# Performance work log

Hardware: AMD Instinct MI355X
Metric: run time of the kernel (lower is better)

Reference implementation:

```python
import jax, jax.numpy as jnp
import numpy as np

BLOCK_SIZE = 16
MASK_TOKEN_ID = 31999
D_MODEL = 2048
N_HEADS = 16
VOCAB = 32000
NEG = -1e30


def setup_inputs() -> dict:
    key = jax.random.key(0)
    ks = jax.random.split(key, 8)
    B, S, D, V = 1, 1024, D_MODEL, VOCAB
    sd = 1.0 / np.sqrt(D)
    return {
        "input_ids": jax.random.randint(ks[0], (B, S), 0, V),
        "attention_mask": jnp.ones((B, S), dtype=jnp.float32),
        "hidden_states": jax.random.normal(ks[1], (B, S, D), dtype=jnp.float32),
        "loss_mask": jnp.ones((B, S), dtype=jnp.float32),
        "embed_table": jax.random.normal(ks[2], (V, D), dtype=jnp.float32) * 0.02,
        "Wq": jax.random.normal(ks[3], (D, D), dtype=jnp.float32) * sd,
        "Wk": jax.random.normal(ks[4], (D, D), dtype=jnp.float32) * sd,
        "Wv": jax.random.normal(ks[5], (D, D), dtype=jnp.float32) * sd,
        "Wo": jax.random.normal(ks[6], (D, D), dtype=jnp.float32) * sd,
        "lm_head_w": jax.random.normal(ks[7], (D, V), dtype=jnp.float32) * sd,
    }


def reference(input_ids, attention_mask, hidden_states, loss_mask,
              embed_table, Wq, Wk, Wv, Wo, lm_head_w):
    B, S = input_ids.shape
    bs = BLOCK_SIZE
    L = (S // bs) * bs  # effective_len
    input_ids = input_ids[:, :L]
    hidden_states = hidden_states[:, :L, :]
    loss_mask = loss_mask[:, :L]

    positions = jnp.arange(L)
    is_block_start = positions % bs == 0
    block_ids = positions // bs

    # noise input: first token of each block real, rest MASK
    noise_ids = jnp.where(is_block_start[None, :], input_ids, MASK_TOKEN_ID)
    noise_emb = embed_table[noise_ids]  # [B, L, D]

    # [L, 2L] DFlash mask: ctx kv visible if its block < q block; noise kv if same block
    ctx_vis = block_ids[None, :] < block_ids[:, None]
    noise_vis = block_ids[:, None] == block_ids[None, :]
    full_mask = jnp.concatenate([ctx_vis, noise_vis], axis=1)  # [L, 2L] bool

    # draft attention: q from noise tokens, kv over [target_hidden ; noise]
    H = N_HEADS
    hd = hidden_states.shape[-1] // H
    kv_in = jnp.concatenate([hidden_states, noise_emb], axis=1)  # [B, 2L, D]
    q = (noise_emb @ Wq).reshape(B, L, H, hd).transpose(0, 2, 1, 3)      # [B,H,L,hd]
    k = (kv_in @ Wk).reshape(B, 2 * L, H, hd).transpose(0, 2, 1, 3)      # [B,H,2L,hd]
    v = (kv_in @ Wv).reshape(B, 2 * L, H, hd).transpose(0, 2, 1, 3)
    scores = jnp.einsum("bhqd,bhkd->bhqk", q, k) / jnp.sqrt(jnp.float32(hd))
    scores = jnp.where(full_mask[None, None, :, :], scores, NEG)
    attn = jax.nn.softmax(scores, axis=-1)
    ctx = jnp.einsum("bhqk,bhkd->bhqd", attn, v)
    hidden = ctx.transpose(0, 2, 1, 3).reshape(B, L, -1) @ Wo  # [B, L, D]

    logits = hidden @ lm_head_w  # [B, L, V]

    # dflash loss mask: exclude first block and block starts (gamma=None)
    is_first_block = block_ids == 0
    valid = (~is_first_block) & (~is_block_start)
    combined = loss_mask * valid.astype(jnp.float32)  # [B, L]
    active = combined > 1e-6

    logp = jax.nn.log_softmax(logits, axis=-1)
    ce = -jnp.take_along_axis(logp, input_ids[..., None], axis=-1)[..., 0]  # [B, L]
    count = jnp.sum(active.astype(jnp.float32))
    loss = jnp.sum(jnp.where(active, ce, 0.0)) / count

    preds = jnp.argmax(logits, axis=-1)
    correct = jnp.sum(jnp.where(active, (preds == input_ids).astype(jnp.float32), 0.0))
    accuracy = correct / count
    return loss, accuracy
```

## Files before the change

kernel.cpp:

```cpp
#include <hip/hip_runtime.h>

typedef unsigned int uint32;
typedef unsigned short u16;
typedef __attribute__((ext_vector_type(8))) short bf16x8;
typedef __attribute__((ext_vector_type(4))) float f32x4;

__device__ __forceinline__ u16 f2b(float f) {
  uint32 u = __float_as_uint(f);
  u = (u + 0x7fffu + ((u >> 16) & 1u)) >> 16;
  return (u16)u;
}
__device__ __forceinline__ float b2f(u16 h) {
  return __uint_as_float(((uint32)h) << 16);
}
__device__ __forceinline__ void gl_lds16(const void* g, void* l) {
  typedef const __attribute__((address_space(1))) void* gp_t;
  typedef __attribute__((address_space(3))) void* lp_t;
  __builtin_amdgcn_global_load_lds((gp_t)g, (lp_t)l, 16, 0, 0);
}

#define L 1024
#define D 2048
#define NH 16
#define HD 128
#define VOCAB 32000
#define KV 2048
#define MASK_ID 31999

static constexpr long OFF_KV  = 0;
static constexpr long OFF_WTQ = OFF_KV  + 8388608;
static constexpr long OFF_WTK = OFF_WTQ + 8388608;
static constexpr long OFF_WTV = OFF_WTK + 8388608;
static constexpr long OFF_WTO = OFF_WTV + 8388608;
static constexpr long OFF_Q   = OFF_WTO + 8388608;
static constexpr long OFF_K   = OFF_Q   + 4194304;
static constexpr long OFF_VT  = OFF_K   + 8388608;
static constexpr long OFF_CTX = OFF_VT  + 8388608;
static constexpr long OFF_HID = OFF_CTX + 4194304;
static constexpr long OFF_LMT = OFF_HID + 4194304;
static constexpr long OFF_PM  = OFF_LMT + 131072000;
static constexpr long OFF_PS  = OFF_PM  + 524288;
static constexpr long OFF_PI  = OFF_PS  + 524288;
static constexpr long OFF_PT  = OFF_PI  + 524288;
static constexpr long OFF_ROW = OFF_PT  + 4096;
static constexpr long WS_NEED = OFF_ROW + 8192;

__global__ __launch_bounds__(256) void prep_kv(const float* __restrict__ hs,
                                               const int* __restrict__ ids,
                                               const float* __restrict__ emb,
                                               u16* __restrict__ kv) {
  int r = blockIdx.x;
  int t = threadIdx.x;
  const float* src;
  if (r < L) {
    src = hs + (long)r * D;
  } else {
    int p = r - L;
    int id = ((p & 15) == 0) ? ids[p] : MASK_ID;
    src = emb + (long)id * D;
  }
  float4 a = *(const float4*)(src + t * 8);
  float4 b = *(const float4*)(src + t * 8 + 4);
  u16* dst = kv + (long)r * D + t * 8;
  ushort4 o0, o1;
  o0.x = f2b(a.x); o0.y = f2b(a.y); o0.z = f2b(a.z); o0.w = f2b(a.w);
  o1.x = f2b(b.x); o1.y = f2b(b.y); o1.z = f2b(b.z); o1.w = f2b(b.w);
  *(ushort4*)dst = o0;
  *(ushort4*)(dst + 4) = o1;
}

__device__ __forceinline__ void transpose_body(const float* __restrict__ W,
                                               u16* __restrict__ WT,
                                               int Kd, int Nd) {
  __shared__ float tile[128 * 129];
  int n0 = blockIdx.x * 128;
  int k0 = blockIdx.y * 128;
  int t = threadIdx.x;
  int r = t >> 5;
  int c4 = (t & 31) * 4;
#pragma unroll
  for (int p = 0; p < 16; ++p) {
    int kk = p * 8 + r;
    float4 v = *(const float4*)(W + (long)(k0 + kk) * Nd + n0 + c4);
    float* dst = tile + kk * 129 + c4;
    dst[0] = v.x; dst[1] = v.y; dst[2] = v.z; dst[3] = v.w;
  }
  __syncthreads();
#pragma unroll
  for (int p = 0; p < 16; ++p) {
    int nn = p * 8 + r;
    ushort4 o;
    o.x = f2b(tile[(c4 + 0) * 129 + nn]);
    o.y = f2b(tile[(c4 + 1) * 129 + nn]);
    o.z = f2b(tile[(c4 + 2) * 129 + nn]);
    o.w = f2b(tile[(c4 + 3) * 129 + nn]);
    *(ushort4*)(WT + (long)(n0 + nn) * Kd + k0 + c4) = o;
  }
}

__global__ __launch_bounds__(256) void transpose_conv(const float* __restrict__ W,
                                                      u16* __restrict__ WT,
                                                      int Kd, int Nd) {
  transpose_body(W, WT, Kd, Nd);
}

__global__ __launch_bounds__(256) void transpose4(const float* __restrict__ W0, const float* __restrict__ W1,
                                                  const float* __restrict__ W2, const float* __restrict__ W3,
                                                  u16* __restrict__ T0, u16* __restrict__ T1,
                                                  u16* __restrict__ T2, u16* __restrict__ T3) {
  int z = blockIdx.z;
  const float* W = (z == 0) ? W0 : (z == 1) ? W1 : (z == 2) ? W2 : W3;
  u16* T = (z == 0) ? T0 : (z == 1) ? T1 : (z == 2) ? T2 : T3;
  transpose_body(W, T, D, D);
}

#define EPI_PLAIN 0
#define EPI_QKV 3
#define EPI_CE 4

template <int EPI>
__global__ __launch_bounds__(256) void gemm128(const u16* __restrict__ A, int lda, long aHead,
                                               const u16* __restrict__ BT, int ldb, long bHead,
                                               u16* __restrict__ C, int ldc, long cHead,
                                               int Kd) {
  __shared__ __align__(16) char lds[16384];
  char* a_lds = lds;
  char* b_lds = lds + 8192;
  int tid = threadIdx.x;
  int lane = tid & 63;
  int wave = tid >> 6;
  int wr = wave >> 1, wc = wave & 1;
  int h = blockIdx.z;
  long tm = (long)blockIdx.x * 128;
  long tn = (long)blockIdx.y * 128;
  const u16* Ap = A + (long)h * aHead + tm * lda;
  const u16* Bp = BT + (long)h * bHead + tn * ldb;

  int soff = tid * 16;
  int srow = soff >> 6;
  int scol = (soff & 63) >> 1;
  char* aldsb = a_lds + wave * 1024;
  char* bldsb = b_lds + wave * 1024;

  f32x4 acc[4][4];
#pragma unroll
  for (int i = 0; i < 4; ++i)
#pragma unroll
    for (int j = 0; j < 4; ++j) acc[i][j] = (f32x4){0.f, 0.f, 0.f, 0.f};

  for (int k0 = 0; k0 < Kd; k0 += 32) {
#pragma unroll
    for (int r = 0; r < 2; ++r) {
      gl_lds16(Ap + (long)(srow + r * 64) * lda + k0 + scol, aldsb + r * 4096);
      gl_lds16(Bp + (long)(srow + r * 64) * ldb + k0 + scol, bldsb + r * 4096);
    }
    __syncthreads();
    bf16x8 af[4], bfr[4];
    int ka = (lane >> 4) << 4;
#pragma unroll
    for (int mi = 0; mi < 4; ++mi)
      af[mi] = *(const bf16x8*)(a_lds + (wr * 64 + mi * 16 + (lane & 15)) * 64 + ka);
#pragma unroll
    for (int ni = 0; ni < 4; ++ni)
      bfr[ni] = *(const bf16x8*)(b_lds + (wc * 64 + ni * 16 + (lane & 15)) * 64 + ka);
#pragma unroll
    for (int mi = 0; mi < 4; ++mi)
#pragma unroll
      for (int ni = 0; ni < 4; ++ni)
        acc[mi][ni] = __builtin_amdgcn_mfma_f32_16x16x32_bf16(af[mi], bfr[ni], acc[mi][ni], 0, 0, 0);
    __syncthreads();
  }

  long crow0 = tm + wr * 64 + ((lane >> 4) << 2);
  int ccol0 = wc * 64 + (lane & 15);
  u16* Cp = C + (long)h * cHead;
#pragma unroll
  for (int mi = 0; mi < 4; ++mi) {
#pragma unroll
    for (int ni = 0; ni < 4; ++ni) {
      long col = tn + ccol0 + ni * 16;
#pragma unroll
      for (int j = 0; j < 4; ++j) {
        long row = crow0 + mi * 16 + j;
        Cp[row * ldc + col] = f2b(acc[mi][ni][j]);
      }
    }
  }
}

template <int EPI>
__global__ __launch_bounds__(512, 2) void gemm256(const u16* __restrict__ A, int lda,
                                                  const u16* __restrict__ BT, int ldb,
                                                  u16* __restrict__ C, int ldc,
                                                  int Kd, int mtiles,
                                                  u16* __restrict__ Cq, u16* __restrict__ Ck,
                                                  u16* __restrict__ Cv,
                                                  const int* __restrict__ ids,
                                                  float* __restrict__ PMAX,
                                                  float* __restrict__ PSUM,
                                                  int* __restrict__ PARGI,
                                                  float* __restrict__ PTGT) {
  __shared__ __align__(16) char lds[131072];
  int nwg = gridDim.x;
  int orig = blockIdx.x;
  int q8 = nwg >> 3, r8 = nwg & 7;
  int xcd = orig & 7, idx = orig >> 3;
  int wg = (xcd < r8 ? xcd * (q8 + 1) : r8 * (q8 + 1) + (xcd - r8) * q8) + idx;
  int tm, tn;
  if (EPI == EPI_QKV) {
    if (wg < 32) { tn = wg >> 2; tm = 4 + (wg & 3); }
    else { int e = wg - 32; tn = 8 + (e >> 3); tm = e & 7; }
  } else {
    tm = wg % mtiles; tn = wg / mtiles;
  }

  int tid = threadIdx.x, lane = tid & 63, w = tid >> 6;
  int wm = w >> 2, wn = w & 3;
  const u16* Ap = A + (long)tm * 256 * lda;
  const u16* Bp = BT + (long)tn * 256 * ldb;
  int NT = Kd >> 6;
  int maxs = NT << 2;

  auto STAGE_SLOT = [&](int s) {
    if (s >= maxs) return;
    int tau = s >> 2, hh = s & 3;
    int kind = (hh & 1) ^ 1;
    int ks = hh >> 1;
    const u16* src = kind ? Bp : Ap;
    int ld = kind ? ldb : lda;
    char* dst0 = lds + (tau & 1) * 65536 + kind * 32768 + ks * 16384;
    long kbase = (long)tau * 64 + ks * 32;
#pragma unroll
    for (int l = 0; l < 2; ++l) {
      int o = tid * 16 + l * 8192;
      int rr = o >> 6;
      int ch = (o >> 4) & 3;
      int clog = ch ^ ((rr >> 1) & 3);
      gl_lds16(src + (long)rr * ld + kbase + clog * 8, dst0 + w * 1024 + l * 8192);
    }
  };
  auto LDA = [&](int tau, int ks, int mi) -> bf16x8 {
    int rr = wm * 128 + mi * 16 + (lane & 15);
    int qq = lane >> 4;
    return *(const bf16x8*)(lds + (tau & 1) * 65536 + ks * 16384 + rr * 64 +
                            ((qq ^ ((rr >> 1) & 3)) << 4));
  };
  auto LDB = [&](int tau, int ks, int ni) -> bf16x8 {
    int rr = wn * 64 + ni * 16 + (lane & 15);
    int qq = lane >> 4;
    return *(const bf16x8*)(lds + (tau & 1) * 65536 + 32768 + ks * 16384 + rr * 64 +
                            ((qq ^ ((rr >> 1) & 3)) << 4));
  };

  f32x4 acc[8][4];
#pragma unroll
  for (int i = 0; i < 8; ++i)
#pragma unroll
    for (int j = 0; j < 4; ++j) acc[i][j] = (f32x4){0.f, 0.f, 0.f, 0.f};

  STAGE_SLOT(0); STAGE_SLOT(1); STAGE_SLOT(2); STAGE_SLOT(3);
  asm volatile("s_waitcnt vmcnt(4)" ::: "memory");
  STAGE_SLOT(4); STAGE_SLOT(5); STAGE_SLOT(6);
  asm volatile("s_waitcnt vmcnt(6)" ::: "memory");
  __builtin_amdgcn_s_barrier();
  __builtin_amdgcn_sched_barrier(0);

  bf16x8 bfr[4];

#define G256_PHASE(TAU, KS, MH, SLOT, WAITV)                                   \
  {                                                                            \
    bf16x8 af[4];                                                              \
    if (MH == 0) {                                                             \
      bfr[0] = LDB(TAU, KS, 0); bfr[1] = LDB(TAU, KS, 1);                      \
      bfr[2] = LDB(TAU, KS, 2); bfr[3] = LDB(TAU, KS, 3);                      \
    }                                                                          \
    af[0] = LDA(TAU, KS, MH * 4 + 0); af[1] = LDA(TAU, KS, MH * 4 + 1);        \
    af[2] = LDA(TAU, KS, MH * 4 + 2); af[3] = LDA(TAU, KS, MH * 4 + 3);        \
    STAGE_SLOT(SLOT);                                                          \
    __builtin_amdgcn_sched_barrier(0);                                         \
    __builtin_amdgcn_s_barrier();                                              \
    asm volatile("s_waitcnt lgkmcnt(0)" ::: "memory");                         \
    __builtin_amdgcn_sched_barrier(0);                                         \
    __builtin_amdgcn_s_setprio(1);                                             \
    _Pragma("unroll")                                                          \
    for (int mi2 = 0; mi2 < 4; ++mi2)                                          \
      _Pragma("unroll")                                                        \
      for (int ni = 0; ni < 4; ++ni)                                           \
        acc[MH * 4 + mi2][ni] = __builtin_amdgcn_mfma_f32_16x16x32_bf16(       \
            af[mi2], bfr[ni], acc[MH * 4 + mi2][ni], 0, 0, 0);                 \
    __builtin_amdgcn_s_setprio(0);                                             \
    __builtin_amdgcn_sched_barrier(0);                                         \
    if (WAITV == 6) asm volatile("s_waitcnt vmcnt(6)" ::: "memory");           \
    else if (WAITV == 0) asm volatile("s_waitcnt vmcnt(0)" ::: "memory");      \
    __builtin_amdgcn_s_barrier();                                              \
    __builtin_amdgcn_sched_barrier(0);                                         \
  }

  for (int t = 0; t < NT; t += 2) {
    int s0 = 4 * t;
    int w4 = (t + 2 >= NT) ? 0 : 6;
    G256_PHASE(t,     0, 0, s0 + 7,  -1)
    G256_PHASE(t,     0, 1, s0 + 8,  -1)
    G256_PHASE(t,     1, 0, s0 + 9,  -1)
    G256_PHASE(t,     1, 1, s0 + 10, w4)
    G256_PHASE(t + 1, 0, 0, s0 + 11, -1)
    G256_PHASE(t + 1, 0, 1, s0 + 12, -1)
    G256_PHASE(t + 1, 1, 0, s0 + 13, -1)
    G256_PHASE(t + 1, 1, 1, s0 + 14, 6)
  }
#undef G256_PHASE

  if (EPI == EPI_CE) {
    __syncthreads();
    float* smax = (float*)lds;
    float* ssum = smax + 1024;
    int* sargi = (int*)(ssum + 1024);
    int lq = lane & 15, qq = lane >> 4;
#pragma unroll
    for (int mi = 0; mi < 8; ++mi) {
#pragma unroll
      for (int j = 0; j < 4; ++j) {
        int lrow = mi * 16 + qq * 4 + j;
        long grow = (long)tm * 256 + wm * 128 + lrow;
        int tgt = ids[grow];
        float v[4];
        float mx = -1e30f; int ai = 0;
#pragma unroll
        for (int ni = 0; ni < 4; ++ni) {
          v[ni] = acc[mi][ni][j];
          int col = tn * 256 + wn * 64 + ni * 16 + lq;
          if (col == tgt) PTGT[grow] = v[ni];
          if (v[ni] > mx) { mx = v[ni]; ai = col; }
        }
#pragma unroll
        for (int off = 1; off < 16; off <<= 1) {
          float om = __shfl_xor(mx, off);
          int oa = __shfl_xor(ai, off);
          if (om > mx || (om == mx && oa < ai)) { mx = om; ai = oa; }
        }
        float se = 0.f;
#pragma unroll
        for (int ni = 0; ni < 4; ++ni) se += __expf(v[ni] - mx);
#pragma unroll
        for (int off = 1; off < 16; off <<= 1) se += __shfl_xor(se, off);
        if (lq == 0) {
          int f = wm * 128 + lrow;
          smax[f * 4 + wn] = mx;
          ssum[f * 4 + wn] = se;
          sargi[f * 4 + wn] = ai;
        }
      }
    }
    __syncthreads();
    if (lane < 32) {
      int f = w * 32 + lane;
      float m_t = smax[f * 4]; int a_t = sargi[f * 4];
#pragma unroll
      for (int x = 1; x < 4; ++x) {
        float om = smax[f * 4 + x]; int oa = sargi[f * 4 + x];
        if (om > m_t || (om == m_t && oa < a_t)) { m_t = om; a_t = oa; }
      }
      float s_t = 0.f;
#pragma unroll
      for (int x = 0; x < 4; ++x) s_t += ssum[f * 4 + x] * __expf(smax[f * 4 + x] - m_t);
      long grow = (long)tm * 256 + f;
      PMAX[grow * 128 + tn] = m_t;
      PSUM[grow * 128 + tn] = s_t;
      PARGI[grow * 128 + tn] = a_t;
    }
    return;
  }

  long crow = (long)tm * 256 + wm * 128 + ((lane >> 4) << 2);
  long ccol = (long)tn * 256 + wn * 64 + (lane & 15);
#pragma unroll
  for (int mi = 0; mi < 8; ++mi)
#pragma unroll
    for (int ni = 0; ni < 4; ++ni)
#pragma unroll
      for (int j = 0; j < 4; ++j) {
        long row = crow + mi * 16 + j;
        long col = ccol + ni * 16;
        u16 val = f2b(acc[mi][ni][j]);
        if (EPI == EPI_PLAIN) {
          C[row * ldc + col] = val;
        } else {
          if (col < 2048) {
            if (row >= 1024) Cq[(row - 1024) * D + col] = val;
          } else if (col < 4096) {
            Ck[row * D + (col - 2048)] = val;
          } else {
            Cv[(col - 4096) * KV + row] = val;
          }
        }
      }
}

__global__ __launch_bounds__(256) void ce_combine(const float* __restrict__ PMAX,
                                                  const float* __restrict__ PSUM,
                                                  const int* __restrict__ PARGI,
                                                  const float* __restrict__ PTGT,
                                                  const int* __restrict__ ids,
                                                  float* __restrict__ rowbuf) {
  int row = blockIdx.x * 4 + (threadIdx.x >> 6);
  int lane = threadIdx.x & 63;
  const float* pm = PMAX + (long)row * 128;
  const float* ps = PSUM + (long)row * 128;
  const int* pi = PARGI + (long)row * 128;
  float m0 = (lane < 125) ? pm[lane] : -1e30f;
  int a0 = (lane < 125) ? pi[lane] : (1 << 30);
  float m1 = (lane + 64 < 125) ? pm[lane + 64] : -1e30f;
  int a1 = (lane + 64 < 125) ? pi[lane + 64] : (1 << 30);
  float mg = m0; int ag = a0;
  if (m1 > mg || (m1 == mg && a1 < ag)) { mg = m1; ag = a1; }
  for (int off = 1; off < 64; off <<= 1) {
    float om = __shfl_xor(mg, off);
    int oa = __shfl_xor(ag, off);
    if (om > mg || (om == mg && oa < ag)) { mg = om; ag = oa; }
  }
  float s = 0.f;
  if (lane < 125) s += ps[lane] * __expf(m0 - mg);
  if (lane + 64 < 125) s += ps[lane + 64] * __expf(m1 - mg);
  for (int off = 1; off < 64; off <<= 1) s += __shfl_xor(s, off);
  if (lane == 0) {
    rowbuf[row * 2] = mg + logf(s) - PTGT[row];
    rowbuf[row * 2 + 1] = (ag == ids[row]) ? 1.f : 0.f;
  }
}

__global__ __launch_bounds__(256) void flash_attn(const u16* __restrict__ qb,
                                                  const u16* __restrict__ kb,
                                                  const u16* __restrict__ vt,
                                                  u16* __restrict__ ctx) {
  int tid = threadIdx.x;
  int lane = tid & 63;
  int wid = blockIdx.x * 4 + (tid >> 6);
  int pairid = wid >> 1;
  int h = pairid >> 5;
  int pr = pairid & 31;
  int rb = (wid & 1) ? (63 - pr) : pr;
  int lq = lane & 15;
  int g = lane >> 4;
  const float scale = 0.08838834764831845f;

  const u16* qrow = qb + (long)(rb * 16 + lq) * D + h * HD + g * 8;
  bf16x8 qf[4];
#pragma unroll
  for (int c = 0; c < 4; ++c) qf[c] = *(const bf16x8*)(qrow + c * 32);

  f32x4 o[8];
#pragma unroll
  for (int i = 0; i < 8; ++i) o[i] = (f32x4){0.f, 0.f, 0.f, 0.f};
  float m = -1e30f, lsum = 0.f;

  int nb = rb + 1;
  for (int bp = 0; bp < nb; bp += 2) {
    bool validB = (bp + 1) < nb;
    int tokA = (bp < rb) ? bp * 16 : 1024 + rb * 16;
    int bB = bp + 1;
    int tokB = validB ? ((bB < rb) ? bB * 16 : 1024 + rb * 16) : tokA;

    f32x4 sA = (f32x4){0.f, 0.f, 0.f, 0.f};
    f32x4 sB = (f32x4){0.f, 0.f, 0.f, 0.f};
    const u16* ka = kb + (long)(tokA + lq) * D + h * HD + g * 8;
#pragma unroll
    for (int c = 0; c < 4; ++c) {
      bf16x8 kf = *(const bf16x8*)(ka + c * 32);
      sA = __builtin_amdgcn_mfma_f32_16x16x32_bf16(kf, qf[c], sA, 0, 0, 0);
    }
    if (validB) {
      const u16* kbp = kb + (long)(tokB + lq) * D + h * HD + g * 8;
#pragma unroll
      for (int c = 0; c < 4; ++c) {
        bf16x8 kf = *(const bf16x8*)(kbp + c * 32);
        sB = __builtin_amdgcn_mfma_f32_16x16x32_bf16(kf, qf[c], sB, 0, 0, 0);
      }
    }

    float s8[8];
#pragma unroll
    for (int j = 0; j < 4; ++j) s8[j] = sA[j] * scale;
#pragma unroll
    for (int j = 0; j < 4; ++j) s8[4 + j] = validB ? sB[j] * scale : -1e30f;
    float mx = s8[0];
#pragma unroll
    for (int j = 1; j < 8; ++j) mx = fmaxf(mx, s8[j]);
    mx = fmaxf(mx, __shfl_xor(mx, 16));
    mx = fmaxf(mx, __shfl_xor(mx, 32));
    float mn = fmaxf(m, mx);
    float sc_f = __expf(m - mn);
    m = mn;
    float p[8], ps = 0.f;
#pragma unroll
    for (int j = 0; j < 8; ++j) { p[j] = __expf(s8[j] - mn); ps += p[j]; }
    ps += __shfl_xor(ps, 16);
    ps += __shfl_xor(ps, 32);
    lsum = lsum * sc_f + ps;

    uint32 Aw0 = (uint32)f2b(p[0]) | ((uint32)f2b(p[1]) << 16);
    uint32 Aw1 = (uint32)f2b(p[2]) | ((uint32)f2b(p[3]) << 16);
    uint32 Bw0 = (uint32)f2b(p[4]) | ((uint32)f2b(p[5]) << 16);
    uint32 Bw1 = (uint32)f2b(p[6]) | ((uint32)f2b(p[7]) << 16);
    int s0 = (((2 * g) & 3) << 4) + lq;
    int s1 = (((2 * g + 1) & 3) << 4) + lq;
    uint32 a00 = (uint32)__shfl((int)Aw0, s0), a01 = (uint32)__shfl((int)Aw1, s0);
    uint32 a10 = (uint32)__shfl((int)Aw0, s1), a11 = (uint32)__shfl((int)Aw1, s1);
    uint32 b00 = (uint32)__shfl((int)Bw0, s0), b01 = (uint32)__shfl((int)Bw1, s0);
    uint32 b10 = (uint32)__shfl((int)Bw0, s1), b11 = (uint32)__shfl((int)Bw1, s1);
    union { uint32 u[4]; bf16x8 v; } pu;
    pu.u[0] = (g < 2) ? a00 : b00;
    pu.u[1] = (g < 2) ? a01 : b01;
    pu.u[2] = (g < 2) ? a10 : b10;
    pu.u[3] = (g < 2) ? a11 : b11;

#pragma unroll
    for (int nt = 0; nt < 8; ++nt)
#pragma unroll
      for (int j = 0; j < 4; ++j) o[nt][j] *= sc_f;
    int tok_g = (g < 2) ? (tokA + g * 8) : (tokB + (g - 2) * 8);
    const u16* vrow = vt + (long)(h * HD + lq) * KV + tok_g;
#pragma unroll
    for (int nt = 0; nt < 8; ++nt) {
      bf16x8 vf = *(const bf16x8*)(vrow + (long)nt * 16 * KV);
      o[nt] = __builtin_amdgcn_mfma_f32_16x16x32_bf16(vf, pu.v, o[nt], 0, 0, 0);
    }
  }

  float inv = 1.f / lsum;
  u16* cp = ctx + (long)(rb * 16 + lq) * D + h * HD + g * 4;
#pragma unroll
  for (int nt = 0; nt < 8; ++nt) {
    ushort4 st;
    st.x = f2b(o[nt][0] * inv); st.y = f2b(o[nt][1] * inv);
    st.z = f2b(o[nt][2] * inv); st.w = f2b(o[nt][3] * inv);
    *(ushort4*)(cp + nt * 16) = st;
  }
}

__global__ __launch_bounds__(256) void final_reduce(const float* __restrict__ rowbuf,
                                                    const float* __restrict__ loss_mask,
                                                    float* __restrict__ out) {
  int t = threadIdx.x;
  float ce = 0.f, cnt = 0.f, cor = 0.f;
  for (int r = t; r < L; r += 256) {
    bool valid = (r >= 16) && ((r & 15) != 0);
    float comb = loss_mask[r] * (valid ? 1.f : 0.f);
    if (comb > 1e-6f) {
      ce += rowbuf[r * 2];
      cor += rowbuf[r * 2 + 1];
      cnt += 1.f;
    }
  }
  for (int off = 1; off < 64; off <<= 1) {
    ce += __shfl_xor(ce, off);
    cnt += __shfl_xor(cnt, off);
    cor += __shfl_xor(cor, off);
  }
  __shared__ float s1[4], s2[4], s3[4];
  int lane = t & 63, w = t >> 6;
  if (lane == 0) { s1[w] = ce; s2[w] = cnt; s3[w] = cor; }
  __syncthreads();
  if (t == 0) {
    float C = s1[0] + s1[1] + s1[2] + s1[3];
    float N = s2[0] + s2[1] + s2[2] + s2[3];
    float R = s3[0] + s3[1] + s3[2] + s3[3];
    out[0] = C / N;
    out[1] = R / N;
  }
}

__global__ void ws_too_small(float* out, float mb) {
  if (threadIdx.x == 0) { out[0] = 1e6f + mb; out[1] = -1e6f; }
}

extern "C" void kernel_launch(void* const* d_in, const int* in_sizes, int n_in,
                              void* d_out, int out_size, void* d_ws, size_t ws_size,
                              hipStream_t stream) {
  const int* ids = (const int*)d_in[0];
  const float* hs = (const float*)d_in[2];
  const float* lmask = (const float*)d_in[3];
  const float* emb = (const float*)d_in[4];
  const float* Wq = (const float*)d_in[5];
  const float* Wk = (const float*)d_in[6];
  const float* Wv = (const float*)d_in[7];
  const float* Wo = (const float*)d_in[8];
  const float* Wlm = (const float*)d_in[9];
  float* out = (float*)d_out;
  char* ws = (char*)d_ws;

  if (ws_size < (size_t)WS_NEED) {
    ws_too_small<<<1, 64, 0, stream>>>(out, (float)(ws_size >> 20));
    return;
  }

  u16* kv  = (u16*)(ws + OFF_KV);
  u16* wtq = (u16*)(ws + OFF_WTQ);
  u16* wtk = (u16*)(ws + OFF_WTK);
  u16* wtv = (u16*)(ws + OFF_WTV);
  u16* wto = (u16*)(ws + OFF_WTO);
  u16* qb  = (u16*)(ws + OFF_Q);
  u16* kb  = (u16*)(ws + OFF_K);
  u16* vt  = (u16*)(ws + OFF_VT);
  u16* ctx = (u16*)(ws + OFF_CTX);
  u16* hid = (u16*)(ws + OFF_HID);
  u16* lmt = (u16*)(ws + OFF_LMT);
  float* PMAX = (float*)(ws + OFF_PM);
  float* PSUM = (float*)(ws + OFF_PS);
  int* PARGI = (int*)(ws + OFF_PI);
  float* PTGT = (float*)(ws + OFF_PT);
  float* rowbuf = (float*)(ws + OFF_ROW);

  prep_kv<<<2048, 256, 0, stream>>>(hs, ids, emb, kv);
  transpose4<<<dim3(16, 16, 4), 256, 0, stream>>>(Wq, Wk, Wv, Wo, wtq, wtk, wtv, wto);
  transpose_conv<<<dim3(250, 16), 256, 0, stream>>>(Wlm, lmt, D, VOCAB);

  gemm256<EPI_QKV><<<dim3(160), 512, 0, stream>>>(kv, D, wtq, D, nullptr, 0, D, 0,
                                                  qb, kb, vt,
                                                  nullptr, nullptr, nullptr, nullptr, nullptr);

  flash_attn<<<dim3(256), 256, 0, stream>>>(qb, kb, vt, ctx);

  gemm128<EPI_PLAIN><<<dim3(8, 16, 1), 256, 0, stream>>>(ctx, D, 0, wto, D, 0, hid, D, 0, D);

  gemm256<EPI_CE><<<dim3(500), 512, 0, stream>>>(hid, D, lmt, D, nullptr, 0, D, 4,
                                                 nullptr, nullptr, nullptr,
                                                 ids, PMAX, PSUM, PARGI, PTGT);

  ce_combine<<<256, 256, 0, stream>>>(PMAX, PSUM, PARGI, PTGT, ids, rowbuf);
  final_reduce<<<1, 256, 0, stream>>>(rowbuf, lmask, out);
}
```

Measured before the change: 465.3 us.

## Merge prep and transposes into one launch, overlap LM-head transpose with QKV GEMM

The kv conversion and the four DxD weight transposes now run in a single 512-thread launch. A second launch runs the QKV GEMM (160 workgroups) alongside a grid-stride transpose of the LM-head weight on the remaining 352 workgroups, so the bandwidth-bound transpose overlaps compute-bound GEMM work. The GEMM body also precomputes its LDS fragment pointers and global staging offsets instead of recomputing addresses in each phase. The costs are idle-block imbalance between the two roles and a 128KB LDS allocation for the transpose blocks, which lowers their occupancy.

```diff
diff --git a/kernel.cpp b/kernel.cpp
--- a/kernel.cpp
+++ b/kernel.cpp
@@ -45,73 +45,70 @@
 static constexpr long OFF_ROW = OFF_PT  + 4096;
 static constexpr long WS_NEED = OFF_ROW + 8192;
 
-__global__ __launch_bounds__(256) void prep_kv(const float* __restrict__ hs,
-                                               const int* __restrict__ ids,
-                                               const float* __restrict__ emb,
-                                               u16* __restrict__ kv) {
-  int r = blockIdx.x;
+__device__ __forceinline__ void transpose128(float* tile, const float* __restrict__ W,
+                                             u16* __restrict__ WT,
+                                             int Kd, int Nd, int k0, int n0) {
   int t = threadIdx.x;
-  const float* src;
-  if (r < L) {
-    src = hs + (long)r * D;
+  int r = t >> 2, cq = (t & 3) * 4;
+#pragma unroll
+  for (int p = 0; p < 8; ++p) {
+    int c = cq + p * 16;
+    float4 v = *(const float4*)(W + (long)(k0 + r) * Nd + n0 + c);
+    float* d = tile + r * 129 + c;
+    d[0] = v.x; d[1] = v.y; d[2] = v.z; d[3] = v.w;
+  }
+  __syncthreads();
+  int q = t & 15, nn0 = t >> 4;
+#pragma unroll
+  for (int p = 0; p < 4; ++p) {
+    int nn = nn0 + p * 32;
+    union { u16 v[8]; bf16x8 b; } u;
+#pragma unroll
+    for (int j = 0; j < 8; ++j) u.v[j] = f2b(tile[(q * 8 + j) * 129 + nn]);
+    *(bf16x8*)(WT + (long)(n0 + nn) * Kd + k0 + q * 8) = u.b;
+  }
+}
+
+__global__ __launch_bounds__(512) void mega1(const float* __restrict__ hs,
+                                             const int* __restrict__ ids,
+                                             const float* __restrict__ emb,
+                                             u16* __restrict__ kv,
+                                             const float* __restrict__ Wq, const float* __restrict__ Wk,
+                                             const float* __restrict__ Wv, const float* __restrict__ Wo,
+                                             u16* __restrict__ wtq, u16* __restrict__ wtk,
+                                             u16* __restrict__ wtv, u16* __restrict__ wto) {
+  __shared__ float tile[128 * 129];
+  int bid = blockIdx.x;
+  int t = threadIdx.x;
+  if (bid < 512) {
+    int r = bid * 4 + (t >> 7);
+    int c0 = (t & 127) * 16;
+    const float* src;
+    if (r < L) {
+      src = hs + (long)r * D;
+    } else {
+      int p = r - L;
+      int id = ((p & 15) == 0) ? ids[p] : MASK_ID;
+      src = emb + (long)id * D;
+    }
+    u16* dst = kv + (long)r * D + c0;
+#pragma unroll
+    for (int qy = 0; qy < 2; ++qy) {
+      float4 a = *(const float4*)(src + c0 + qy * 8);
+      float4 b = *(const float4*)(src + c0 + qy * 8 + 4);
+      ushort4 o0, o1;
+      o0.x = f2b(a.x); o0.y = f2b(a.y); o0.z = f2b(a.z); o0.w = f2b(a.w);
+      o1.x = f2b(b.x); o1.y = f2b(b.y); o1.z = f2b(b.z); o1.w = f2b(b.w);
+      *(ushort4*)(dst + qy * 8) = o0;
+      *(ushort4*)(dst + qy * 8 + 4) = o1;
+    }
   } else {
-    int p = r - L;
-    int id = ((p & 15) == 0) ? ids[p] : MASK_ID;
-    src = emb + (long)id * D;
-  }
-  float4 a = *(const float4*)(src + t * 8);
-  float4 b = *(const float4*)(src + t * 8 + 4);
-  u16* dst = kv + (long)r * D + t * 8;
-  ushort4 o0, o1;
-  o0.x = f2b(a.x); o0.y = f2b(a.y); o0.z = f2b(a.z); o0.w = f2b(a.w);
-  o1.x = f2b(b.x); o1.y = f2b(b.y); o1.z = f2b(b.z); o1.w = f2b(b.w);
-  *(ushort4*)dst = o0;
-  *(ushort4*)(dst + 4) = o1;
-}
-
-__device__ __forceinline__ void transpose_body(const float* __restrict__ W,
-                                               u16* __restrict__ WT,
-                                               int Kd, int Nd) {
-  __shared__ float tile[128 * 129];
-  int n0 = blockIdx.x * 128;
-  int k0 = blockIdx.y * 128;
-  int t = threadIdx.x;
-  int r = t >> 5;
-  int c4 = (t & 31) * 4;
-#pragma unroll
-  for (int p = 0; p < 16; ++p) {
-    int kk = p * 8 + r;
-    float4 v = *(const float4*)(W + (long)(k0 + kk) * Nd + n0 + c4);
-    float* dst = tile + kk * 129 + c4;
-    dst[0] = v.x; dst[1] = v.y; dst[2] = v.z; dst[3] = v.w;
-  }
-  __syncthreads();
-#pragma unroll
-  for (int p = 0; p < 16; ++p) {
-    int nn = p * 8 + r;
-    ushort4 o;
-    o.x = f2b(tile[(c4 + 0) * 129 + nn]);
-    o.y = f2b(tile[(c4 + 1) * 129 + nn]);
-    o.z = f2b(tile[(c4 + 2) * 129 + nn]);
-    o.w = f2b(tile[(c4 + 3) * 129 + nn]);
-    *(ushort4*)(WT + (long)(n0 + nn) * Kd + k0 + c4) = o;
-  }
-}
-
-__global__ __launch_bounds__(256) void transpose_conv(const float* __restrict__ W,
-                                                      u16* __restrict__ WT,
-                                                      int Kd, int Nd) {
-  transpose_body(W, WT, Kd, Nd);
-}
-
-__global__ __launch_bounds__(256) void transpose4(const float* __restrict__ W0, const float* __restrict__ W1,
-                                                  const float* __restrict__ W2, const float* __restrict__ W3,
-                                                  u16* __restrict__ T0, u16* __restrict__ T1,
-                                                  u16* __restrict__ T2, u16* __restrict__ T3) {
-  int z = blockIdx.z;
-  const float* W = (z == 0) ? W0 : (z == 1) ? W1 : (z == 2) ? W2 : W3;
-  u16* T = (z == 0) ? T0 : (z == 1) ? T1 : (z == 2) ? T2 : T3;
-  transpose_body(W, T, D, D);
+    int idx = bid - 512;
+    int z = idx >> 8, tt = idx & 255;
+    const float* W = (z == 0) ? Wq : (z == 1) ? Wk : (z == 2) ? Wv : Wo;
+    u16* T = (z == 0) ? wtq : (z == 1) ? wtk : (z == 2) ? wtv : wto;
+    transpose128(tile, W, T, D, D, (tt >> 4) * 128, (tt & 15) * 128);
+  }
 }
 
 #define EPI_PLAIN 0
@@ -189,23 +186,15 @@
 }
 
 template <int EPI>
-__global__ __launch_bounds__(512, 2) void gemm256(const u16* __restrict__ A, int lda,
-                                                  const u16* __restrict__ BT, int ldb,
-                                                  u16* __restrict__ C, int ldc,
-                                                  int Kd, int mtiles,
-                                                  u16* __restrict__ Cq, u16* __restrict__ Ck,
-                                                  u16* __restrict__ Cv,
-                                                  const int* __restrict__ ids,
-                                                  float* __restrict__ PMAX,
-                                                  float* __restrict__ PSUM,
-                                                  int* __restrict__ PARGI,
-                                                  float* __restrict__ PTGT) {
-  __shared__ __align__(16) char lds[131072];
-  int nwg = gridDim.x;
-  int orig = blockIdx.x;
-  int q8 = nwg >> 3, r8 = nwg & 7;
-  int xcd = orig & 7, idx = orig >> 3;
-  int wg = (xcd < r8 ? xcd * (q8 + 1) : r8 * (q8 + 1) + (xcd - r8) * q8) + idx;
+__device__ __forceinline__ void gemm256_body(char* lds, int wg,
+                                             const u16* __restrict__ A, int lda,
+                                             const u16* __restrict__ BT,
+                                             int Kd, int mtiles,
+                                             u16* __restrict__ Cq, u16* __restrict__ Ck,
+                                             u16* __restrict__ Cv,
+                                             const int* __restrict__ ids,
+                                             float* __restrict__ PMAX, float* __restrict__ PSUM,
+                                             int* __restrict__ PARGI, float* __restrict__ PTGT) {
   int tm, tn;
   if (EPI == EPI_QKV) {
     if (wg < 32) { tn = wg >> 2; tm = 4 + (wg & 3); }
@@ -216,40 +205,39 @@
 
   int tid = threadIdx.x, lane = tid & 63, w = tid >> 6;
   int wm = w >> 2, wn = w & 3;
-  const u16* Ap = A + (long)tm * 256 * lda;
-  const u16* Bp = BT + (long)tn * 256 * ldb;
+  int lq = lane & 15, qq = lane >> 4;
+  const char* Ap = (const char*)(A + (long)tm * 256 * lda);
+  const char* Bp = (const char*)(BT + (long)tn * 256 * lda);
   int NT = Kd >> 6;
   int maxs = NT << 2;
+
+  int swz = qq ^ ((lq >> 1) & 3);
+  char* pA0 = lds + ((wm * 128 + lq) * 64 + (swz << 4));
+  char* pA1 = pA0 + 65536;
+  char* pB0 = lds + 32768 + ((wn * 64 + lq) * 64 + (swz << 4));
+  char* pB1 = pB0 + 65536;
+  int voff[2], lof[2];
+#pragma unroll
+  for (int l = 0; l < 2; ++l) {
+    int o = tid * 16 + l * 8192;
+    int rr = o >> 6;
+    int ch = (o >> 4) & 3;
+    int clog = ch ^ ((rr >> 1) & 3);
+    voff[l] = (rr * lda + clog * 8) * 2;
+    lof[l] = w * 1024 + l * 8192;
+  }
 
   auto STAGE_SLOT = [&](int s) {
     if (s >= maxs) return;
     int tau = s >> 2, hh = s & 3;
     int kind = (hh & 1) ^ 1;
     int ks = hh >> 1;
-    const u16* src = kind ? Bp : Ap;
-    int ld = kind ? ldb : lda;
-    char* dst0 = lds + (tau & 1) * 65536 + kind * 32768 + ks * 16384;
-    long kbase = (long)tau * 64 + ks * 32;
-#pragma unroll
-    for (int l = 0; l < 2; ++l) {
-      int o = tid * 16 + l * 8192;
-      int rr = o >> 6;
-      int ch = (o >> 4) & 3;
-      int clog = ch ^ ((rr >> 1) & 3);
-      gl_lds16(src + (long)rr * ld + kbase + clog * 8, dst0 + w * 1024 + l * 8192);
-    }
-  };
-  auto LDA = [&](int tau, int ks, int mi) -> bf16x8 {
-    int rr = wm * 128 + mi * 16 + (lane & 15);
-    int qq = lane >> 4;
-    return *(const bf16x8*)(lds + (tau & 1) * 65536 + ks * 16384 + rr * 64 +
-                            ((qq ^ ((rr >> 1) & 3)) << 4));
-  };
-  auto LDB = [&](int tau, int ks, int ni) -> bf16x8 {
-    int rr = wn * 64 + ni * 16 + (lane & 15);
-    int qq = lane >> 4;
-    return *(const bf16x8*)(lds + (tau & 1) * 65536 + 32768 + ks * 16384 + rr * 64 +
-                            ((qq ^ ((rr >> 1) & 3)) << 4));
+    const char* src = kind ? Bp : Ap;
+    long kb = (long)tau * 128 + ks * 64;
+    char* dstb = lds + (tau & 1) * 65536 + kind * 32768 + ks * 16384;
+#pragma unroll
+    for (int l = 0; l < 2; ++l)
+      gl_lds16(src + kb + voff[l], dstb + lof[l]);
   };
 
   f32x4 acc[8][4];
@@ -267,15 +255,19 @@
 
   bf16x8 bfr[4];
 
-#define G256_PHASE(TAU, KS, MH, SLOT, WAITV)                                   \
+#define G256_PHASE(PA, PB, KS, MH, SLOT, WAITV)                                \
   {                                                                            \
     bf16x8 af[4];                                                              \
     if (MH == 0) {                                                             \
-      bfr[0] = LDB(TAU, KS, 0); bfr[1] = LDB(TAU, KS, 1);                      \
-      bfr[2] = LDB(TAU, KS, 2); bfr[3] = LDB(TAU, KS, 3);                      \
+      bfr[0] = *(const bf16x8*)((PB) + (KS) * 16384 + 0 * 1024);               \
+      bfr[1] = *(const bf16x8*)((PB) + (KS) * 16384 + 1 * 1024);               \
+      bfr[2] = *(const bf16x8*)((PB) + (KS) * 16384 + 2 * 1024);               \
+      bfr[3] = *(const bf16x8*)((PB) + (KS) * 16384 + 3 * 1024);               \
     }                                                                          \
-    af[0] = LDA(TAU, KS, MH * 4 + 0); af[1] = LDA(TAU, KS, MH * 4 + 1);        \
-    af[2] = LDA(TAU, KS, MH * 4 + 2); af[3] = LDA(TAU, KS, MH * 4 + 3);        \
+    af[0] = *(const bf16x8*)((PA) + (KS) * 16384 + (MH * 4 + 0) * 1024);       \
+    af[1] = *(const bf16x8*)((PA) + (KS) * 16384 + (MH * 4 + 1) * 1024);       \
+    af[2] = *(const bf16x8*)((PA) + (KS) * 16384 + (MH * 4 + 2) * 1024);       \
+    af[3] = *(const bf16x8*)((PA) + (KS) * 16384 + (MH * 4 + 3) * 1024);       \
     STAGE_SLOT(SLOT);                                                          \
     __builtin_amdgcn_sched_barrier(0);                                         \
     __builtin_amdgcn_s_barrier();                                              \
@@ -299,14 +291,14 @@
   for (int t = 0; t < NT; t += 2) {
     int s0 = 4 * t;
     int w4 = (t + 2 >= NT) ? 0 : 6;
-    G256_PHASE(t,     0, 0, s0 + 7,  -1)
-    G256_PHASE(t,     0, 1, s0 + 8,  -1)
-    G256_PHASE(t,     1, 0, s0 + 9,  -1)
-    G256_PHASE(t,     1, 1, s0 + 10, w4)
-    G256_PHASE(t + 1, 0, 0, s0 + 11, -1)
-    G256_PHASE(t + 1, 0, 1, s0 + 12, -1)
-    G256_PHASE(t + 1, 1, 0, s0 + 13, -1)
-    G256_PHASE(t + 1, 1, 1, s0 + 14, 6)
+    G256_PHASE(pA0, pB0, 0, 0, s0 + 7,  -1)
+    G256_PHASE(pA0, pB0, 0, 1, s0 + 8,  -1)
+    G256_PHASE(pA0, pB0, 1, 0, s0 + 9,  -1)
+    G256_PHASE(pA0, pB0, 1, 1, s0 + 10, w4)
+    G256_PHASE(pA1, pB1, 0, 0, s0 + 11, -1)
+    G256_PHASE(pA1, pB1, 0, 1, s0 + 12, -1)
+    G256_PHASE(pA1, pB1, 1, 0, s0 + 13, -1)
+    G256_PHASE(pA1, pB1, 1, 1, s0 + 14, 6)
   }
 #undef G256_PHASE
 
@@ -315,7 +307,6 @@
     float* smax = (float*)lds;
     float* ssum = smax + 1024;
     int* sargi = (int*)(ssum + 1024);
-    int lq = lane & 15, qq = lane >> 4;
 #pragma unroll
     for (int mi = 0; mi < 8; ++mi) {
 #pragma unroll
@@ -372,7 +363,7 @@
   }
 
   long crow = (long)tm * 256 + wm * 128 + ((lane >> 4) << 2);
-  long ccol = (long)tn * 256 + wn * 64 + (lane & 15);
+  long ccol = (long)tn * 256 + wn * 64 + lq;
 #pragma unroll
   for (int mi = 0; mi < 8; ++mi)
 #pragma unroll
@@ -382,18 +373,51 @@
         long row = crow + mi * 16 + j;
         long col = ccol + ni * 16;
         u16 val = f2b(acc[mi][ni][j]);
-        if (EPI == EPI_PLAIN) {
-          C[row * ldc + col] = val;
+        if (col < 2048) {
+          if (row >= 1024) Cq[(row - 1024) * D + col] = val;
+        } else if (col < 4096) {
+          Ck[row * D + (col - 2048)] = val;
         } else {
-          if (col < 2048) {
-            if (row >= 1024) Cq[(row - 1024) * D + col] = val;
-          } else if (col < 4096) {
-            Ck[row * D + (col - 2048)] = val;
-          } else {
-            Cv[(col - 4096) * KV + row] = val;
-          }
+          Cv[(col - 4096) * KV + row] = val;
         }
       }
+}
+
+__global__ __launch_bounds__(512, 2) void mega2(const u16* __restrict__ kv,
+                                                const u16* __restrict__ wtq,
+                                                u16* __restrict__ qb, u16* __restrict__ kb,
+                                                u16* __restrict__ vt,
+                                                const float* __restrict__ Wlm,
+                                                u16* __restrict__ lmt) {
+  __shared__ __align__(16) char lds[131072];
+  int bid = blockIdx.x;
+  if (bid < 160) {
+    int wg = (bid & 7) * 20 + (bid >> 3);
+    gemm256_body<EPI_QKV>(lds, wg, kv, D, wtq, D, 0, qb, kb, vt,
+                          nullptr, nullptr, nullptr, nullptr, nullptr);
+  } else {
+    for (int tile = bid - 160; tile < 4000; tile += 352) {
+      int n0 = (tile % 250) * 128;
+      int k0 = (tile / 250) * 128;
+      transpose128((float*)lds, Wlm, lmt, D, VOCAB, k0, n0);
+      __syncthreads();
+    }
+  }
+}
+
+__global__ __launch_bounds__(512, 2) void gemm256_ce(const u16* __restrict__ A,
+                                                     const u16* __restrict__ BT,
+                                                     const int* __restrict__ ids,
+                                                     float* __restrict__ PMAX, float* __restrict__ PSUM,
+                                                     int* __restrict__ PARGI, float* __restrict__ PTGT) {
+  __shared__ __align__(16) char lds[131072];
+  int nwg = gridDim.x;
+  int orig = blockIdx.x;
+  int q8 = nwg >> 3, r8 = nwg & 7;
+  int xcd = orig & 7, idx = orig >> 3;
+  int wg = (xcd < r8 ? xcd * (q8 + 1) : r8 * (q8 + 1) + (xcd - r8) * q8) + idx;
+  gemm256_body<EPI_CE>(lds, wg, A, D, BT, D, 4, nullptr, nullptr, nullptr,
+                       ids, PMAX, PSUM, PARGI, PTGT);
 }
 
 __global__ __launch_bounds__(256) void ce_combine(const float* __restrict__ PMAX,
@@ -610,21 +634,15 @@
   float* PTGT = (float*)(ws + OFF_PT);
   float* rowbuf = (float*)(ws + OFF_ROW);
 
-  prep_kv<<<2048, 256, 0, stream>>>(hs, ids, emb, kv);
-  transpose4<<<dim3(16, 16, 4), 256, 0, stream>>>(Wq, Wk, Wv, Wo, wtq, wtk, wtv, wto);
-  transpose_conv<<<dim3(250, 16), 256, 0, stream>>>(Wlm, lmt, D, VOCAB);
-
-  gemm256<EPI_QKV><<<dim3(160), 512, 0, stream>>>(kv, D, wtq, D, nullptr, 0, D, 0,
-                                                  qb, kb, vt,
-                                                  nullptr, nullptr, nullptr, nullptr, nullptr);
+  mega1<<<dim3(1536), 512, 0, stream>>>(hs, ids, emb, kv, Wq, Wk, Wv, Wo,
+                                        wtq, wtk, wtv, wto);
+  mega2<<<dim3(512), 512, 0, stream>>>(kv, wtq, qb, kb, vt, Wlm, lmt);
 
   flash_attn<<<dim3(256), 256, 0, stream>>>(qb, kb, vt, ctx);
 
   gemm128<EPI_PLAIN><<<dim3(8, 16, 1), 256, 0, stream>>>(ctx, D, 0, wto, D, 0, hid, D, 0, D);
 
-  gemm256<EPI_CE><<<dim3(500), 512, 0, stream>>>(hid, D, lmt, D, nullptr, 0, D, 4,
-                                                 nullptr, nullptr, nullptr,
-                                                 ids, PMAX, PSUM, PARGI, PTGT);
+  gemm256_ce<<<dim3(500), 512, 0, stream>>>(hid, lmt, ids, PMAX, PSUM, PARGI, PTGT);
 
   ce_combine<<<256, 256, 0, stream>>>(PMAX, PSUM, PARGI, PTGT, ids, rowbuf);
   final_reduce<<<1, 256, 0, stream>>>(rowbuf, lmask, out);
```

Result: faster. 439.6 us (median of 2 runs) (-5.5%).
